# Performance work log

Hardware: AMD Instinct MI355X
Metric: run time of the kernel (lower is better)

The kernel has to match this reference:

```python
import jax, jax.numpy as jnp
import numpy as np

H = 100  # hidden size of both LSTM layers (fixed in the module)

def lstm_layer(x, w_ih, w_hh, b_ih, b_hh):
    # x: [B, T, I]; w_ih: [4H, I]; w_hh: [4H, H]; biases: [4H]
    # PyTorch gate order: input, forget, cell(g), output.
    B, T, _ = x.shape
    xg = jnp.einsum('bti,gi->btg', x, w_ih) + b_ih + b_hh  # [B, T, 4H], input GEMM hoisted out of the scan
    h0 = jnp.zeros((B, H), x.dtype)
    c0 = jnp.zeros((B, H), x.dtype)
    w_hh_t = w_hh.T  # [H, 4H]

    def step(carry, xg_t):
        h, c = carry
        g = xg_t + h @ w_hh_t                # [B, 4H]
        i, f, gg, o = jnp.split(g, 4, axis=-1)
        i = jax.nn.sigmoid(i)
        f = jax.nn.sigmoid(f)
        gg = jnp.tanh(gg)
        o = jax.nn.sigmoid(o)
        c = f * c + i * gg
        h = o * jnp.tanh(c)
        return (h, c), h

    _, hs = jax.lax.scan(step, (h0, c0), jnp.swapaxes(xg, 0, 1))  # hs: [T, B, H]
    return jnp.swapaxes(hs, 0, 1)  # [B, T, H]


def setup_inputs() -> dict:
    key = jax.random.key(0)
    ks = jax.random.split(key, 13)
    B, T, I = 256, 2048, 8
    s = lambda fan: 1.0 / np.sqrt(fan)
    u = lambda k, shape, fan: jax.random.uniform(k, shape, jnp.float32, -s(fan), s(fan))
    return {
        'x': jax.random.normal(ks[0], (B, T, I), jnp.float32),
        'w_ih1': u(ks[1], (4 * H, I), H), 'w_hh1': u(ks[2], (4 * H, H), H),
        'b_ih1': u(ks[3], (4 * H,), H), 'b_hh1': u(ks[4], (4 * H,), H),
        'w_ih2': u(ks[5], (4 * H, H), H), 'w_hh2': u(ks[6], (4 * H, H), H),
        'b_ih2': u(ks[7], (4 * H,), H), 'b_hh2': u(ks[8], (4 * H,), H),
        'fc1_w': u(ks[9], (25, H), H), 'fc1_b': u(ks[10], (25,), H),
        'fc2_w': u(ks[11], (1, 25), 25), 'fc2_b': u(ks[12], (1,), 25),
    }


def reference(x, w_ih1, w_hh1, b_ih1, b_hh1, w_ih2, w_hh2, b_ih2, b_hh2,
              fc1_w, fc1_b, fc2_w, fc2_b):
    # Dropout layers are identity in eval mode.
    h1 = lstm_layer(x, w_ih1, w_hh1, b_ih1, b_hh1)    # [B, T, H]
    h2 = lstm_layer(h1, w_ih2, w_hh2, b_ih2, b_hh2)   # [B, T, H]
    last = h2[:, -1, :]                               # [B, H]
    y = last @ fc1_w.T + fc1_b                        # [B, 25]
    return y @ fc2_w.T + fc2_b                        # [B, 1]
```

## Files before the change

kernel.cpp:

```cpp
#include <hip/hip_runtime.h>

#define BB 256
#define TT 2048
#define HD 100
#define NG 400

typedef _Float16 h2v __attribute__((ext_vector_type(2)));

__device__ __forceinline__ float fdot2u(unsigned a, unsigned b, float c) {
#if __has_builtin(__builtin_amdgcn_fdot2)
    return __builtin_amdgcn_fdot2(__builtin_bit_cast(h2v, a),
                                  __builtin_bit_cast(h2v, b), c, false);
#else
    h2v av = __builtin_bit_cast(h2v, a), bv = __builtin_bit_cast(h2v, b);
    c = fmaf((float)av[0], (float)bv[0], c);
    c = fmaf((float)av[1], (float)bv[1], c);
    return c;
#endif
}
__device__ __forceinline__ unsigned packh2(float a, float b) {
    h2v p; p[0] = (_Float16)a; p[1] = (_Float16)b;
    return __builtin_bit_cast(unsigned, p);
}
__device__ __forceinline__ float sigmoid_f(float x) {
    return 1.0f / (1.0f + __expf(-x));
}
__device__ __forceinline__ float tanh_f(float x) {
    return 1.0f - 2.0f / (__expf(2.0f * x) + 1.0f);
}

__global__ __launch_bounds__(896, 4) void lstm_fused(
    const float* __restrict__ x,
    const float* __restrict__ w_ih1, const float* __restrict__ w_hh1,
    const float* __restrict__ b_ih1, const float* __restrict__ b_hh1,
    const float* __restrict__ w_ih2, const float* __restrict__ w_hh2,
    const float* __restrict__ b_ih2, const float* __restrict__ b_hh2,
    const float* __restrict__ fc1_w, const float* __restrict__ fc1_b,
    const float* __restrict__ fc2_w, const float* __restrict__ fc2_b,
    float* __restrict__ out)
{
    const int b   = blockIdx.x;
    const int tid = threadIdx.x;

    __shared__ __align__(16) unsigned h1p[52];
    __shared__ __align__(16) unsigned h2p[52];
    __shared__ __align__(16) unsigned xb[2][32][4];
    __shared__ float g1[NG];
    __shared__ float g2[NG];
    __shared__ float h2f[HD];
    __shared__ float fca[25];

    const bool isG1 = (tid < NG);
    const int  g2i  = tid - 448;
    const bool isG2 = (g2i >= 0 && g2i < NG);
    const bool isLd = (tid >= 400 && tid < 432);
    const bool isU1 = (tid < HD);
    const bool isU2 = (g2i >= 0 && g2i < HD);

    unsigned wa[52], wb[52];
    unsigned wx[4];
    float bias = 0.0f, c = 0.0f;

    if (isG1) {
        const float4* ip = (const float4*)(w_ih1 + (size_t)tid * 8);
        float4 v0 = ip[0], v1 = ip[1];
        wx[0] = packh2(v0.x, v0.y); wx[1] = packh2(v0.z, v0.w);
        wx[2] = packh2(v1.x, v1.y); wx[3] = packh2(v1.z, v1.w);
        const float4* hp = (const float4*)(w_hh1 + (size_t)tid * HD);
        #pragma unroll
        for (int k2 = 0; k2 < 25; ++k2) {
            float4 v = hp[k2];
            wa[2*k2]   = packh2(v.x, v.y);
            wa[2*k2+1] = packh2(v.z, v.w);
        }
        wa[50] = 0u; wa[51] = 0u;
        bias = b_ih1[tid] + b_hh1[tid];
    }
    if (isG2) {
        const float4* ip = (const float4*)(w_ih2 + (size_t)g2i * HD);
        const float4* hp = (const float4*)(w_hh2 + (size_t)g2i * HD);
        #pragma unroll
        for (int k2 = 0; k2 < 25; ++k2) {
            float4 v = ip[k2];
            wa[2*k2]   = packh2(v.x, v.y);
            wa[2*k2+1] = packh2(v.z, v.w);
        }
        #pragma unroll
        for (int k2 = 0; k2 < 25; ++k2) {
            float4 v = hp[k2];
            wb[2*k2]   = packh2(v.x, v.y);
            wb[2*k2+1] = packh2(v.z, v.w);
        }
        wa[50] = wa[51] = wb[50] = wb[51] = 0u;
        bias = b_ih2[g2i] + b_hh2[g2i];
    }

    if (tid < 52) h1p[tid] = 0u;
    else if (tid >= 64 && tid < 116) h2p[tid - 64] = 0u;
    if (isLd) {
        const int s = tid - 400;
        const float4* xp = (const float4*)(x + ((size_t)b * TT + s) * 8);
        float4 a0 = xp[0], a1 = xp[1];
        xb[0][s][0] = packh2(a0.x, a0.y); xb[0][s][1] = packh2(a0.z, a0.w);
        xb[0][s][2] = packh2(a1.x, a1.y); xb[0][s][3] = packh2(a1.z, a1.w);
    }
    __syncthreads();

    float4 pa = {0,0,0,0}, pb = {0,0,0,0};

    #pragma unroll 1
    for (int i = 0; i <= TT; ++i) {
        const bool pf = ((i & 31) == 0) && (i + 32 < TT);
        if (isG1 && i < TT) {
            const unsigned* xq = xb[(i >> 5) & 1][i & 31];
            float a0 = bias, a1 = 0.0f;
            a0 = fdot2u(wx[0], xq[0], a0);
            a1 = fdot2u(wx[1], xq[1], a1);
            a0 = fdot2u(wx[2], xq[2], a0);
            a1 = fdot2u(wx[3], xq[3], a1);
            #pragma unroll
            for (int cI = 0; cI < 13; ++cI) {
                uint4 hv = ((const uint4*)h1p)[cI];
                a0 = fdot2u(wa[4*cI+0], hv.x, a0);
                a1 = fdot2u(wa[4*cI+1], hv.y, a1);
                a0 = fdot2u(wa[4*cI+2], hv.z, a0);
                a1 = fdot2u(wa[4*cI+3], hv.w, a1);
            }
            float acc = a0 + a1;
            g1[tid] = (tid < 200 || tid >= 300) ? sigmoid_f(acc) : tanh_f(acc);
        }
        if (isLd && pf) {
            const float4* xp = (const float4*)(x + ((size_t)b * TT + (i + 32) + (tid - 400)) * 8);
            pa = xp[0]; pb = xp[1];
        }
        if (isG2 && i >= 1) {
            float a0 = bias, a1 = 0.0f;
            #pragma unroll
            for (int cI = 0; cI < 13; ++cI) {
                uint4 hv = ((const uint4*)h1p)[cI];
                a0 = fdot2u(wa[4*cI+0], hv.x, a0);
                a1 = fdot2u(wa[4*cI+1], hv.y, a1);
                a0 = fdot2u(wa[4*cI+2], hv.z, a0);
                a1 = fdot2u(wa[4*cI+3], hv.w, a1);
            }
            #pragma unroll
            for (int cI = 0; cI < 13; ++cI) {
                uint4 hv = ((const uint4*)h2p)[cI];
                a0 = fdot2u(wb[4*cI+0], hv.x, a0);
                a1 = fdot2u(wb[4*cI+1], hv.y, a1);
                a0 = fdot2u(wb[4*cI+2], hv.z, a0);
                a1 = fdot2u(wb[4*cI+3], hv.w, a1);
            }
            float acc = a0 + a1;
            g2[g2i] = (g2i < 200 || g2i >= 300) ? sigmoid_f(acc) : tanh_f(acc);
        }
        __syncthreads();
        if (isU1 && i < TT) {
            float gi = g1[tid], gf = g1[HD + tid], gg = g1[2*HD + tid], go = g1[3*HD + tid];
            c = gf * c + gi * gg;
            float h = go * tanh_f(c);
            reinterpret_cast<_Float16*>(h1p)[tid] = (_Float16)h;
        }
        if (isU2 && i >= 1) {
            float gi = g2[g2i], gf = g2[HD + g2i], gg = g2[2*HD + g2i], go = g2[3*HD + g2i];
            c = gf * c + gi * gg;
            float h = go * tanh_f(c);
            reinterpret_cast<_Float16*>(h2p)[g2i] = (_Float16)h;
            if (i == TT) h2f[g2i] = h;
        }
        if (isLd && pf) {
            const int s  = tid - 400;
            const int nb = ((i >> 5) + 1) & 1;
            xb[nb][s][0] = packh2(pa.x, pa.y); xb[nb][s][1] = packh2(pa.z, pa.w);
            xb[nb][s][2] = packh2(pb.x, pb.y); xb[nb][s][3] = packh2(pb.z, pb.w);
        }
        __syncthreads();
    }

    if (tid < 25) {
        float a = fc1_b[tid];
        const float* wp = fc1_w + tid * HD;
        #pragma unroll
        for (int k = 0; k < HD; ++k) a += h2f[k] * wp[k];
        fca[tid] = a;
    }
    __syncthreads();
    if (tid == 0) {
        float y = fc2_b[0];
        #pragma unroll
        for (int m = 0; m < 25; ++m) y += fca[m] * fc2_w[m];
        out[b] = y;
    }
}

extern "C" void kernel_launch(void* const* d_in, const int* in_sizes, int n_in,
                              void* d_out, int out_size, void* d_ws, size_t ws_size,
                              hipStream_t stream) {
    const float* x     = (const float*)d_in[0];
    const float* w_ih1 = (const float*)d_in[1];
    const float* w_hh1 = (const float*)d_in[2];
    const float* b_ih1 = (const float*)d_in[3];
    const float* b_hh1 = (const float*)d_in[4];
    const float* w_ih2 = (const float*)d_in[5];
    const float* w_hh2 = (const float*)d_in[6];
    const float* b_ih2 = (const float*)d_in[7];
    const float* b_hh2 = (const float*)d_in[8];
    const float* fc1_w = (const float*)d_in[9];
    const float* fc1_b = (const float*)d_in[10];
    const float* fc2_w = (const float*)d_in[11];
    const float* fc2_b = (const float*)d_in[12];
    float* out = (float*)d_out;

    lstm_fused<<<BB, 896, 0, stream>>>(x, w_ih1, w_hh1, b_ih1, b_hh1,
                                       w_ih2, w_hh2, b_ih2, b_hh2,
                                       fc1_w, fc1_b, fc2_w, fc2_b, out);
}
```

Before: 2.923 ms.

## Broadcast hidden state via readlane and pad gate rows to wave-aligned blocks

```diff
diff --git a/kernel.cpp b/kernel.cpp
--- a/kernel.cpp
+++ b/kernel.cpp
@@ -3,16 +3,16 @@
 #define BB 256
 #define TT 2048
 #define HD 100
-#define NG 400
+#define NGP 448
 
 typedef _Float16 h2v __attribute__((ext_vector_type(2)));
 
-__device__ __forceinline__ float fdot2u(unsigned a, unsigned b, float c) {
+__device__ __forceinline__ float fdot2s(unsigned w, unsigned h, float c) {
 #if __has_builtin(__builtin_amdgcn_fdot2)
-    return __builtin_amdgcn_fdot2(__builtin_bit_cast(h2v, a),
-                                  __builtin_bit_cast(h2v, b), c, false);
+    return __builtin_amdgcn_fdot2(__builtin_bit_cast(h2v, w),
+                                  __builtin_bit_cast(h2v, h), c, false);
 #else
-    h2v av = __builtin_bit_cast(h2v, a), bv = __builtin_bit_cast(h2v, b);
+    h2v av = __builtin_bit_cast(h2v, w), bv = __builtin_bit_cast(h2v, h);
     c = fmaf((float)av[0], (float)bv[0], c);
     c = fmaf((float)av[1], (float)bv[1], c);
     return c;
@@ -29,7 +29,7 @@
     return 1.0f - 2.0f / (__expf(2.0f * x) + 1.0f);
 }
 
-__global__ __launch_bounds__(896, 4) void lstm_fused(
+__global__ __launch_bounds__(960, 1) void lstm_fused(
     const float* __restrict__ x,
     const float* __restrict__ w_ih1, const float* __restrict__ w_hh1,
     const float* __restrict__ b_ih1, const float* __restrict__ b_hh1,
@@ -39,70 +39,79 @@
     const float* __restrict__ fc2_w, const float* __restrict__ fc2_b,
     float* __restrict__ out)
 {
-    const int b   = blockIdx.x;
-    const int tid = threadIdx.x;
-
-    __shared__ __align__(16) unsigned h1p[52];
-    __shared__ __align__(16) unsigned h2p[52];
+    const int b    = blockIdx.x;
+    const int tid  = threadIdx.x;
+    const int lane = tid & 63;
+
+    __shared__ unsigned h1p[64];
+    __shared__ unsigned h2p[64];
     __shared__ __align__(16) unsigned xb[2][32][4];
-    __shared__ float g1[NG];
-    __shared__ float g2[NG];
+    __shared__ float g1[NGP];
+    __shared__ float g2[NGP];
     __shared__ float h2f[HD];
     __shared__ float fca[25];
 
-    const bool isG1 = (tid < NG);
-    const int  g2i  = tid - 448;
-    const bool isG2 = (g2i >= 0 && g2i < NG);
-    const bool isLd = (tid >= 400 && tid < 432);
-    const bool isU1 = (tid < HD);
-    const bool isU2 = (g2i >= 0 && g2i < HD);
-
-    unsigned wa[52], wb[52];
+    const bool isL1 = (tid < NGP);
+    const bool isL2 = (tid >= NGP && tid < 2 * NGP);
+    const bool isLd = (tid >= 896 && tid < 928);
+    const bool isU1 = (tid < 50);
+    const int  u2m  = tid - NGP;
+    const bool isU2 = (u2m >= 0 && u2m < 50);
+
+    const int g    = isL2 ? (tid - NGP) : tid;
+    const int blk  = g / 112;
+    const int r    = g - blk * 112;
+    const int srow = blk * HD + r;
+    const bool real = (isL1 || isL2) && (r < HD);
+
     unsigned wx[4];
-    float bias = 0.0f, c = 0.0f;
-
-    if (isG1) {
-        const float4* ip = (const float4*)(w_ih1 + (size_t)tid * 8);
+    unsigned wa[50], wb[50];
+    float bias = 0.0f;
+    float c0 = 0.0f, c1 = 0.0f;
+
+    wx[0] = wx[1] = wx[2] = wx[3] = 0u;
+    #pragma unroll
+    for (int q = 0; q < 50; ++q) { wa[q] = 0u; wb[q] = 0u; }
+
+    if (isL1 && real) {
+        const float4* ip = (const float4*)(w_ih1 + (size_t)srow * 8);
         float4 v0 = ip[0], v1 = ip[1];
         wx[0] = packh2(v0.x, v0.y); wx[1] = packh2(v0.z, v0.w);
         wx[2] = packh2(v1.x, v1.y); wx[3] = packh2(v1.z, v1.w);
-        const float4* hp = (const float4*)(w_hh1 + (size_t)tid * HD);
-        #pragma unroll
-        for (int k2 = 0; k2 < 25; ++k2) {
-            float4 v = hp[k2];
-            wa[2*k2]   = packh2(v.x, v.y);
-            wa[2*k2+1] = packh2(v.z, v.w);
-        }
-        wa[50] = 0u; wa[51] = 0u;
-        bias = b_ih1[tid] + b_hh1[tid];
-    }
-    if (isG2) {
-        const float4* ip = (const float4*)(w_ih2 + (size_t)g2i * HD);
-        const float4* hp = (const float4*)(w_hh2 + (size_t)g2i * HD);
-        #pragma unroll
-        for (int k2 = 0; k2 < 25; ++k2) {
-            float4 v = ip[k2];
-            wa[2*k2]   = packh2(v.x, v.y);
-            wa[2*k2+1] = packh2(v.z, v.w);
-        }
-        #pragma unroll
-        for (int k2 = 0; k2 < 25; ++k2) {
-            float4 v = hp[k2];
-            wb[2*k2]   = packh2(v.x, v.y);
-            wb[2*k2+1] = packh2(v.z, v.w);
-        }
-        wa[50] = wa[51] = wb[50] = wb[51] = 0u;
-        bias = b_ih2[g2i] + b_hh2[g2i];
-    }
-
-    if (tid < 52) h1p[tid] = 0u;
-    else if (tid >= 64 && tid < 116) h2p[tid - 64] = 0u;
+        const float4* hp = (const float4*)(w_hh1 + (size_t)srow * HD);
+        #pragma unroll
+        for (int q = 0; q < 25; ++q) {
+            float4 v = hp[q];
+            wa[2*q]   = packh2(v.x, v.y);
+            wa[2*q+1] = packh2(v.z, v.w);
+        }
+        bias = b_ih1[srow] + b_hh1[srow];
+    }
+    if (isL2 && real) {
+        const float4* ip = (const float4*)(w_ih2 + (size_t)srow * HD);
+        #pragma unroll
+        for (int q = 0; q < 25; ++q) {
+            float4 v = ip[q];
+            wa[2*q]   = packh2(v.x, v.y);
+            wa[2*q+1] = packh2(v.z, v.w);
+        }
+        const float4* hp = (const float4*)(w_hh2 + (size_t)srow * HD);
+        #pragma unroll
+        for (int q = 0; q < 25; ++q) {
+            float4 v = hp[q];
+            wb[2*q]   = packh2(v.x, v.y);
+            wb[2*q+1] = packh2(v.z, v.w);
+        }
+        bias = b_ih2[srow] + b_hh2[srow];
+    }
+
+    if (tid < 64) { h1p[tid] = 0u; h2p[tid] = 0u; }
     if (isLd) {
-        const int s = tid - 400;
+        const int s = tid - 896;
         const float4* xp = (const float4*)(x + ((size_t)b * TT + s) * 8);
-        float4 a0 = xp[0], a1 = xp[1];
-        xb[0][s][0] = packh2(a0.x, a0.y); xb[0][s][1] = packh2(a0.z, a0.w);
-        xb[0][s][2] = packh2(a1.x, a1.y); xb[0][s][3] = packh2(a1.z, a1.w);
+        float4 a0v = xp[0], a1v = xp[1];
+        xb[0][s][0] = packh2(a0v.x, a0v.y); xb[0][s][1] = packh2(a0v.z, a0v.w);
+        xb[0][s][2] = packh2(a1v.x, a1v.y); xb[0][s][3] = packh2(a1v.z, a1v.w);
     }
     __syncthreads();
 
@@ -111,65 +120,74 @@
     #pragma unroll 1
     for (int i = 0; i <= TT; ++i) {
         const bool pf = ((i & 31) == 0) && (i + 32 < TT);
-        if (isG1 && i < TT) {
-            const unsigned* xq = xb[(i >> 5) & 1][i & 31];
+        if (isL1 && i < TT) {
+            unsigned st = h1p[lane];
+            const uint4 xq = *((const uint4*)xb[(i >> 5) & 1][i & 31]);
             float a0 = bias, a1 = 0.0f;
-            a0 = fdot2u(wx[0], xq[0], a0);
-            a1 = fdot2u(wx[1], xq[1], a1);
-            a0 = fdot2u(wx[2], xq[2], a0);
-            a1 = fdot2u(wx[3], xq[3], a1);
+            a0 = fdot2s(wx[0], xq.x, a0);
+            a1 = fdot2s(wx[1], xq.y, a1);
+            a0 = fdot2s(wx[2], xq.z, a0);
+            a1 = fdot2s(wx[3], xq.w, a1);
             #pragma unroll
-            for (int cI = 0; cI < 13; ++cI) {
-                uint4 hv = ((const uint4*)h1p)[cI];
-                a0 = fdot2u(wa[4*cI+0], hv.x, a0);
-                a1 = fdot2u(wa[4*cI+1], hv.y, a1);
-                a0 = fdot2u(wa[4*cI+2], hv.z, a0);
-                a1 = fdot2u(wa[4*cI+3], hv.w, a1);
+            for (int k = 0; k < 50; ++k) {
+                unsigned hk = (unsigned)__builtin_amdgcn_readlane((int)st, k);
+                if (k & 1) a1 = fdot2s(wa[k], hk, a1);
+                else       a0 = fdot2s(wa[k], hk, a0);
             }
             float acc = a0 + a1;
-            g1[tid] = (tid < 200 || tid >= 300) ? sigmoid_f(acc) : tanh_f(acc);
+            g1[g] = (blk == 2) ? tanh_f(acc) : sigmoid_f(acc);
         }
         if (isLd && pf) {
-            const float4* xp = (const float4*)(x + ((size_t)b * TT + (i + 32) + (tid - 400)) * 8);
+            const float4* xp = (const float4*)(x + ((size_t)b * TT + (i + 32) + (tid - 896)) * 8);
             pa = xp[0]; pb = xp[1];
         }
-        if (isG2 && i >= 1) {
+        if (isL2 && i >= 1) {
+            unsigned st1 = h1p[lane];
+            unsigned st2 = h2p[lane];
             float a0 = bias, a1 = 0.0f;
             #pragma unroll
-            for (int cI = 0; cI < 13; ++cI) {
-                uint4 hv = ((const uint4*)h1p)[cI];
-                a0 = fdot2u(wa[4*cI+0], hv.x, a0);
-                a1 = fdot2u(wa[4*cI+1], hv.y, a1);
-                a0 = fdot2u(wa[4*cI+2], hv.z, a0);
-                a1 = fdot2u(wa[4*cI+3], hv.w, a1);
+            for (int k = 0; k < 50; ++k) {
+                unsigned hk = (unsigned)__builtin_amdgcn_readlane((int)st1, k);
+                if (k & 1) a1 = fdot2s(wa[k], hk, a1);
+                else       a0 = fdot2s(wa[k], hk, a0);
             }
             #pragma unroll
-            for (int cI = 0; cI < 13; ++cI) {
-                uint4 hv = ((const uint4*)h2p)[cI];
-                a0 = fdot2u(wb[4*cI+0], hv.x, a0);
-                a1 = fdot2u(wb[4*cI+1], hv.y, a1);
-                a0 = fdot2u(wb[4*cI+2], hv.z, a0);
-                a1 = fdot2u(wb[4*cI+3], hv.w, a1);
+            for (int k = 0; k < 50; ++k) {
+                unsigned hk = (unsigned)__builtin_amdgcn_readlane((int)st2, k);
+                if (k & 1) a1 = fdot2s(wb[k], hk, a1);
+                else       a0 = fdot2s(wb[k], hk, a0);
             }
             float acc = a0 + a1;
-            g2[g2i] = (g2i < 200 || g2i >= 300) ? sigmoid_f(acc) : tanh_f(acc);
+            g2[g] = (blk == 2) ? tanh_f(acc) : sigmoid_f(acc);
         }
         __syncthreads();
         if (isU1 && i < TT) {
-            float gi = g1[tid], gf = g1[HD + tid], gg = g1[2*HD + tid], go = g1[3*HD + tid];
-            c = gf * c + gi * gg;
-            float h = go * tanh_f(c);
-            reinterpret_cast<_Float16*>(h1p)[tid] = (_Float16)h;
+            const int m = tid;
+            float2 iv = *(const float2*)(g1 + 2*m);
+            float2 fv = *(const float2*)(g1 + 112 + 2*m);
+            float2 gv = *(const float2*)(g1 + 224 + 2*m);
+            float2 ov = *(const float2*)(g1 + 336 + 2*m);
+            c0 = fv.x * c0 + iv.x * gv.x;
+            c1 = fv.y * c1 + iv.y * gv.y;
+            float h0 = ov.x * tanh_f(c0);
+            float h1 = ov.y * tanh_f(c1);
+            h1p[m] = packh2(h0, h1);
         }
         if (isU2 && i >= 1) {
-            float gi = g2[g2i], gf = g2[HD + g2i], gg = g2[2*HD + g2i], go = g2[3*HD + g2i];
-            c = gf * c + gi * gg;
-            float h = go * tanh_f(c);
-            reinterpret_cast<_Float16*>(h2p)[g2i] = (_Float16)h;
-            if (i == TT) h2f[g2i] = h;
+            const int m = u2m;
+            float2 iv = *(const float2*)(g2 + 2*m);
+            float2 fv = *(const float2*)(g2 + 112 + 2*m);
+            float2 gv = *(const float2*)(g2 + 224 + 2*m);
+            float2 ov = *(const float2*)(g2 + 336 + 2*m);
+            c0 = fv.x * c0 + iv.x * gv.x;
+            c1 = fv.y * c1 + iv.y * gv.y;
+            float h0 = ov.x * tanh_f(c0);
+            float h1 = ov.y * tanh_f(c1);
+            h2p[m] = packh2(h0, h1);
+            if (i == TT) { h2f[2*m] = h0; h2f[2*m+1] = h1; }
         }
         if (isLd && pf) {
-            const int s  = tid - 400;
+            const int s  = tid - 896;
             const int nb = ((i >> 5) + 1) & 1;
             xb[nb][s][0] = packh2(pa.x, pa.y); xb[nb][s][1] = packh2(pa.z, pa.w);
             xb[nb][s][2] = packh2(pb.x, pb.y); xb[nb][s][3] = packh2(pb.z, pb.w);
@@ -211,7 +229,7 @@
     const float* fc2_b = (const float*)d_in[12];
     float* out = (float*)d_out;
 
-    lstm_fused<<<BB, 896, 0, stream>>>(x, w_ih1, w_hh1, b_ih1, b_hh1,
+    lstm_fused<<<BB, 960, 0, stream>>>(x, w_ih1, w_hh1, b_ih1, b_hh1,
                                        w_ih2, w_hh2, b_ih2, b_hh2,
                                        fc1_w, fc1_b, fc2_w, fc2_b, out);
 }
```

Result: slower. 3.393 ms (+16.1%).
